# Kernel tuning notes

Hardware: AMD Instinct MI355X
Metric: run time of the kernel (lower is better)

Reference implementation:

```python
import jax, jax.numpy as jnp
import numpy as np

K = 3  # three_nn
EPS = 1e-10


def setup_inputs() -> dict:
    key = jax.random.key(0)
    ks = jax.random.split(key, 10)
    B, N, NP = 4, 16384, 4096
    C1, C2 = 128, 256
    Cin, H1, H2, Cout = C1 + C2, 256, 256, 128
    xyz1 = jax.random.normal(ks[0], (B, N, 3), dtype=jnp.float32)
    xyz2 = jax.random.normal(ks[1], (B, NP, 3), dtype=jnp.float32)
    features1 = jax.random.normal(ks[2], (B, N, C1), dtype=jnp.float32)
    features2 = jax.random.normal(ks[3], (B, NP, C2), dtype=jnp.float32)
    def lin(k, fan_in, fan_out):
        bound = 1.0 / np.sqrt(fan_in)
        kw, kb = jax.random.split(k)
        W = jax.random.uniform(kw, (fan_in, fan_out), jnp.float32, -bound, bound)
        b = jax.random.uniform(kb, (fan_out,), jnp.float32, -bound, bound)
        return W, b
    W1, b1 = lin(ks[4], Cin, H1)
    W2, b2 = lin(ks[5], H1, H2)
    W3, b3 = lin(ks[6], H2, Cout)
    return {"xyz1": xyz1, "xyz2": xyz2, "features1": features1,
            "features2": features2, "W1": W1, "b1": b1, "W2": W2,
            "b2": b2, "W3": W3, "b3": b3}


def _three_nn(xyz1, xyz2):
    # squared pairwise distances via |a|^2 + |b|^2 - 2 a.b  -> [B, N, npoint]
    sq1 = jnp.sum(xyz1 * xyz1, axis=-1)  # [B, N]
    sq2 = jnp.sum(xyz2 * xyz2, axis=-1)  # [B, npoint]
    dots = jnp.einsum("bnd,bmd->bnm", xyz1, xyz2)
    sqdist = sq1[:, :, None] + sq2[:, None, :] - 2.0 * dots
    neg_d, idx = jax.lax.top_k(-sqdist, K)  # 3 smallest squared distances
    return -neg_d, idx  # dist:[B,N,3], idx:[B,N,3]


def reference(xyz1, xyz2, features1, features2, W1, b1, W2, b2, W3, b3):
    B = xyz1.shape[0]
    dist, idx = _three_nn(xyz1, xyz2)
    # torch custom three_nn is non-differentiable in dist
    dist = jax.lax.stop_gradient(dist)
    dist = jnp.maximum(dist, EPS)
    recip = 1.0 / dist                                  # [B, N, 3]
    weight = recip / jnp.sum(recip, axis=-1, keepdims=True)
    # three_interpolate: gather neighbor features and weighted-sum
    batch_idx = jnp.arange(B)[:, None, None]
    gathered = features2[batch_idx, idx]                # [B, N, 3, C2]
    interp = jnp.einsum("bnkc,bnk->bnc", gathered, weight)
    new_features = jnp.concatenate([features1, interp], axis=-1)
    h = jax.nn.relu(new_features @ W1 + b1)
    h = jax.nn.relu(h @ W2 + b2)
    return h @ W3 + b3
```

## Files before the change

kernel.cpp:

```cpp
#include <hip/hip_runtime.h>
#include <stdint.h>

#define QT   65536
#define NPTS 4096
#define C1   128
#define C2   256
#define CIN  384
#define COUT 128

typedef _Float16 f16;
typedef __attribute__((ext_vector_type(8))) _Float16 f16x8;
typedef __attribute__((ext_vector_type(4))) float f32x4;

__device__ __attribute__((aligned(16))) f16 g_w1p[12 * 16 * 64 * 8];
__device__ __attribute__((aligned(16))) f16 g_w2p[8 * 16 * 64 * 8];
__device__ __attribute__((aligned(16))) f16 g_w3p[8 * 8 * 64 * 8];
__device__ __attribute__((aligned(16))) float4 g_cand[4 * NPTS];

__device__ inline void packW4(const float* __restrict__ W, f16* __restrict__ dst,
                              int i, int N, int NCB) {
  const int g = i & 3, quad = (i >> 2) & 3, cbk = i >> 4;
  const int cb = cbk % NCB, kcb = cbk / NCB;
  const int col = cb * 16 + g * 4;
  const int k0 = kcb * 32 + quad * 8;
  f16x8 o[4];
#pragma unroll
  for (int e = 0; e < 8; ++e) {
    float4 v = *(const float4*)(W + (size_t)(k0 + e) * N + col);
    o[0][e] = (f16)v.x; o[1][e] = (f16)v.y; o[2][e] = (f16)v.z; o[3][e] = (f16)v.w;
  }
  f16* base = dst + ((size_t)cbk * 64 + quad * 16 + g * 4) * 8;
#pragma unroll
  for (int j = 0; j < 4; ++j) *(f16x8*)(base + j * 8) = o[j];
}

__global__ __launch_bounds__(256) void prep(
    const float* __restrict__ xyz2, const float* __restrict__ W1,
    const float* __restrict__ W2,   const float* __restrict__ W3) {
  const int tid = blockIdx.x * 256 + threadIdx.x;
  const int nthr = gridDim.x * 256;
  for (int i = tid; i < 4 * NPTS; i += nthr) {
    const float* p = xyz2 + (size_t)i * 3;
    float x = p[0], y = p[1], z = p[2];
    g_cand[i] = make_float4(x, y, z, fmaf(x, x, fmaf(y, y, z * z)));
  }
  for (int i = tid; i < 12 * 16 * 16; i += nthr) packW4(W1, g_w1p, i, 256, 16);
  for (int i = tid; i < 8 * 16 * 16; i += nthr) packW4(W2, g_w2p, i, 256, 16);
  for (int i = tid; i < 8 * 8 * 16; i += nthr) packW4(W3, g_w3p, i, 128, 8);
}

__device__ inline uint32_t umin(uint32_t a, uint32_t b) { return a < b ? a : b; }
__device__ inline uint32_t med3u(uint32_t a, uint32_t b, uint32_t c) {
  uint32_t d;
  asm("v_med3_u32 %0, %1, %2, %3" : "=v"(d) : "v"(a), "v"(b), "v"(c));
  return d;
}

#define XS_STRIDE 392
#define HS_STRIDE 264
#define DMPD_OFF 16384
#define DMPI_OFF 28672
#define WV_OFF 50176
#define IV_OFF 51200
#define SMEM_BYTES 52224

__global__ __launch_bounds__(512) void fused_fp(
    const float* __restrict__ xyz1, const float* __restrict__ xyz2,
    const float* __restrict__ f1,   const float* __restrict__ f2,
    const float* __restrict__ W1,   const float* __restrict__ b1,
    const float* __restrict__ W2,   const float* __restrict__ b2,
    const float* __restrict__ W3,   const float* __restrict__ b3,
    float* __restrict__ out)
{
  __shared__ __align__(16) char smem[SMEM_BYTES];
  double*   dmpD = (double*)(smem + DMPD_OFF);
  int*      dmpI = (int*)(smem + DMPI_OFF);
  float*    wvp  = (float*)(smem + WV_OFF);
  int*      ivp  = (int*)(smem + IV_OFF);
  f16*      Xs   = (f16*)smem;
  f16*      Hs   = (f16*)smem;

  const int t = threadIdx.x;
  const int r = t & 63;
  const int w = t >> 6;
  const int qb = blockIdx.x * 64;
  const int batch = qb >> 14;
  const float* xz2b = xyz2 + (size_t)batch * NPTS * 3;
  const float* f2b  = f2   + (size_t)batch * NPTS * C2;

  const int q = qb + r;
  const float qx = xyz1[q * 3], qy = xyz1[q * 3 + 1], qz = xyz1[q * 3 + 2];
  const float nx = -2.f * qx, ny = -2.f * qy, nz = -2.f * qz;
  const float sq1q = qx * qx + qy * qy + qz * qz;

  uint32_t k0 = ~0u, k1 = ~0u, k2 = ~0u, k3 = ~0u, k4 = ~0u;

  auto ins5 = [&](uint32_t c) {
    uint32_t n0 = umin(k0, c);
    uint32_t n1 = med3u(k0, k1, c);
    uint32_t n2 = med3u(k1, k2, c);
    uint32_t n3 = med3u(k2, k3, c);
    uint32_t n4 = med3u(k3, k4, c);
    k0 = n0; k1 = n1; k2 = n2; k3 = n3; k4 = n4;
  };
  auto packk = [&](float e, uint32_t idx) -> uint32_t {
    return (__builtin_bit_cast(uint32_t, e) & 0xFFFFF000u) | idx;
  };

  {
    const int wu = __builtin_amdgcn_readfirstlane(w);
    const float4* __restrict__ cp = g_cand + (batch << 12) + (wu << 9);
    const uint32_t abase = (uint32_t)(wu << 9);
    const float sbias = sq1q + 0.05f;
    #pragma unroll 2
    for (int m = 0; m < 512; m += 4) {
      float4 c0 = cp[m], c1 = cp[m + 1], c2 = cp[m + 2], c3 = cp[m + 3];
      float e0 = fmaf(nx, c0.x, fmaf(ny, c0.y, fmaf(nz, c0.z, c0.w + sbias)));
      float e1 = fmaf(nx, c1.x, fmaf(ny, c1.y, fmaf(nz, c1.z, c1.w + sbias)));
      float e2 = fmaf(nx, c2.x, fmaf(ny, c2.y, fmaf(nz, c2.z, c2.w + sbias)));
      float e3 = fmaf(nx, c3.x, fmaf(ny, c3.y, fmaf(nz, c3.z, c3.w + sbias)));
      ins5(packk(e0, abase + m));
      ins5(packk(e1, abase + m + 1));
      ins5(packk(e2, abase + m + 2));
      ins5(packk(e3, abase + m + 3));
    }
  }

  {
    const double x1 = (double)qx, y1 = (double)qy, z1 = (double)qz;
    const double sq1 = x1 * x1 + y1 * y1 + z1 * z1;
    double d0 = 1e300, d1 = 1e300, d2 = 1e300;
    int j0 = 0, j1 = 0, j2 = 0;
    uint32_t sv[5] = {k0, k1, k2, k3, k4};
    #pragma unroll
    for (int s = 0; s < 5; ++s) {
      int idx = (int)(sv[s] & (NPTS - 1));
      const float* p2 = xz2b + (size_t)idx * 3;
      double x2 = (double)p2[0], y2 = (double)p2[1], z2 = (double)p2[2];
      double d = sq1 + (x2 * x2 + y2 * y2 + z2 * z2)
                     - 2.0 * (x1 * x2 + y1 * y2 + z1 * z2);
      bool c2 = (d < d2) || (d == d2 && idx < j2);
      bool c1 = (d < d1) || (d == d1 && idx < j1);
      bool c0 = (d < d0) || (d == d0 && idx < j0);
      d2 = c1 ? d1 : (c2 ? d : d2);  j2 = c1 ? j1 : (c2 ? idx : j2);
      d1 = c0 ? d0 : (c1 ? d : d1);  j1 = c0 ? j0 : (c1 ? idx : j1);
      d0 = c0 ? d : d0;              j0 = c0 ? idx : j0;
    }
    const int base = (w * 64 + r) * 3;
    dmpD[base]     = d0;  dmpI[base]     = j0;
    dmpD[base + 1] = d1;  dmpI[base + 1] = j1;
    dmpD[base + 2] = d2;  dmpI[base + 2] = j2;
  }
  __syncthreads();

  if (w == 0) {
    double d0 = 1e300, d1 = 1e300, d2 = 1e300;
    int j0 = 0, j1 = 0, j2 = 0;
    #pragma unroll
    for (int w2 = 0; w2 < 8; ++w2) {
      #pragma unroll
      for (int s = 0; s < 3; ++s) {
        const int base = (w2 * 64 + r) * 3 + s;
        double d = dmpD[base];
        int idx  = dmpI[base];
        bool c2 = (d < d2) || (d == d2 && idx < j2);
        bool c1 = (d < d1) || (d == d1 && idx < j1);
        bool c0 = (d < d0) || (d == d0 && idx < j0);
        d2 = c1 ? d1 : (c2 ? d : d2);  j2 = c1 ? j1 : (c2 ? idx : j2);
        d1 = c0 ? d0 : (c1 ? d : d1);  j1 = c0 ? j0 : (c1 ? idx : j1);
        d0 = c0 ? d : d0;              j0 = c0 ? idx : j0;
      }
    }
    float e0 = fmaxf((float)d0, 1e-10f);
    float e1 = fmaxf((float)d1, 1e-10f);
    float e2 = fmaxf((float)d2, 1e-10f);
    float r0 = 1.f / e0, r1 = 1.f / e1, r2 = 1.f / e2;
    float inv = 1.f / (r0 + r1 + r2);
    wvp[r * 4 + 0] = r0 * inv; wvp[r * 4 + 1] = r1 * inv;
    wvp[r * 4 + 2] = r2 * inv; wvp[r * 4 + 3] = 0.f;
    ivp[r * 4 + 0] = j0; ivp[r * 4 + 1] = j1; ivp[r * 4 + 2] = j2; ivp[r * 4 + 3] = 0;
  }
  __syncthreads();

  {
    const int row = t >> 3, c = t & 7;
    f16* xr = Xs + row * XS_STRIDE;
    {
      const float* f1r = f1 + (size_t)(qb + row) * C1 + c * 16;
      float4 u0 = *(const float4*)(f1r);
      float4 u1 = *(const float4*)(f1r + 4);
      float4 u2 = *(const float4*)(f1r + 8);
      float4 u3 = *(const float4*)(f1r + 12);
      f16x8 o0, o1;
      o0[0] = (f16)u0.x; o0[1] = (f16)u0.y; o0[2] = (f16)u0.z; o0[3] = (f16)u0.w;
      o0[4] = (f16)u1.x; o0[5] = (f16)u1.y; o0[6] = (f16)u1.z; o0[7] = (f16)u1.w;
      o1[0] = (f16)u2.x; o1[1] = (f16)u2.y; o1[2] = (f16)u2.z; o1[3] = (f16)u2.w;
      o1[4] = (f16)u3.x; o1[5] = (f16)u3.y; o1[6] = (f16)u3.z; o1[7] = (f16)u3.w;
      *(f16x8*)(xr + c * 16)     = o0;
      *(f16x8*)(xr + c * 16 + 8) = o1;
    }
    const float w0 = wvp[row * 4 + 0], w1 = wvp[row * 4 + 1], w2 = wvp[row * 4 + 2];
    const float* p0 = f2b + (size_t)(ivp[row * 4 + 0] & (NPTS - 1)) * C2;
    const float* p1 = f2b + (size_t)(ivp[row * 4 + 1] & (NPTS - 1)) * C2;
    const float* p2 = f2b + (size_t)(ivp[row * 4 + 2] & (NPTS - 1)) * C2;
    #pragma unroll
    for (int ch = 0; ch < 4; ++ch) {
      const int col = ch * 64 + c * 8;
      float4 a0 = *(const float4*)(p0 + col), b0 = *(const float4*)(p0 + col + 4);
      float4 a1 = *(const float4*)(p1 + col), b1v = *(const float4*)(p1 + col + 4);
      float4 a2 = *(const float4*)(p2 + col), b2v = *(const float4*)(p2 + col + 4);
      f16x8 o;
      o[0] = (f16)(w0 * a0.x + w1 * a1.x + w2 * a2.x);
      o[1] = (f16)(w0 * a0.y + w1 * a1.y + w2 * a2.y);
      o[2] = (f16)(w0 * a0.z + w1 * a1.z + w2 * a2.z);
      o[3] = (f16)(w0 * a0.w + w1 * a1.w + w2 * a2.w);
      o[4] = (f16)(w0 * b0.x + w1 * b1v.x + w2 * b2v.x);
      o[5] = (f16)(w0 * b0.y + w1 * b1v.y + w2 * b2v.y);
      o[6] = (f16)(w0 * b0.z + w1 * b1v.z + w2 * b2v.z);
      o[7] = (f16)(w0 * b0.w + w1 * b1v.w + w2 * b2v.w);
      *(f16x8*)(xr + C1 + col) = o;
    }
  }
  __syncthreads();

  const int l16 = r & 15, quad = r >> 4;
  const int nb = w * 32;

  f32x4 acc[4][2];
  #pragma unroll
  for (int i = 0; i < 4; ++i)
    #pragma unroll
    for (int j = 0; j < 2; ++j) acc[i][j] = f32x4{0.f, 0.f, 0.f, 0.f};

  #pragma unroll
  for (int kc = 0; kc < CIN; kc += 32) {
    f16x8 a[4];
    #pragma unroll
    for (int i = 0; i < 4; ++i)
      a[i] = *(const f16x8*)(Xs + (i * 16 + l16) * XS_STRIDE + kc + quad * 8);
    f16x8 b[2];
    #pragma unroll
    for (int j = 0; j < 2; ++j)
      b[j] = *((const f16x8*)g_w1p +
               (size_t)((kc >> 5) * 16 + (w * 2 + j)) * 64 + r);
    #pragma unroll
    for (int i = 0; i < 4; ++i)
      #pragma unroll
      for (int j = 0; j < 2; ++j)
        acc[i][j] = __builtin_amdgcn_mfma_f32_16x16x32_f16(a[i], b[j], acc[i][j], 0, 0, 0);
  }
  __syncthreads();
  #pragma unroll
  for (int j = 0; j < 2; ++j) {
    float bv = b1[nb + j * 16 + l16];
    #pragma unroll
    for (int i = 0; i < 4; ++i)
      #pragma unroll
      for (int e = 0; e < 4; ++e) {
        int row = i * 16 + quad * 4 + e;
        Hs[row * HS_STRIDE + nb + j * 16 + l16] =
            (f16)fmaxf(acc[i][j][e] + bv, 0.f);
      }
  }
  __syncthreads();

  f32x4 acc2[4][2];
  #pragma unroll
  for (int i = 0; i < 4; ++i)
    #pragma unroll
    for (int j = 0; j < 2; ++j) acc2[i][j] = f32x4{0.f, 0.f, 0.f, 0.f};

  #pragma unroll
  for (int kc = 0; kc < 256; kc += 32) {
    f16x8 a[4];
    #pragma unroll
    for (int i = 0; i < 4; ++i)
      a[i] = *(const f16x8*)(Hs + (i * 16 + l16) * HS_STRIDE + kc + quad * 8);
    f16x8 b[2];
    #pragma unroll
    for (int j = 0; j < 2; ++j)
      b[j] = *((const f16x8*)g_w2p +
               (size_t)((kc >> 5) * 16 + (w * 2 + j)) * 64 + r);
    #pragma unroll
    for (int i = 0; i < 4; ++i)
      #pragma unroll
      for (int j = 0; j < 2; ++j)
        acc2[i][j] = __builtin_amdgcn_mfma_f32_16x16x32_f16(a[i], b[j], acc2[i][j], 0, 0, 0);
  }
  __syncthreads();
  #pragma unroll
  for (int j = 0; j < 2; ++j) {
    float bv = b2[nb + j * 16 + l16];
    #pragma unroll
    for (int i = 0; i < 4; ++i)
      #pragma unroll
      for (int e = 0; e < 4; ++e) {
        int row = i * 16 + quad * 4 + e;
        Hs[row * HS_STRIDE + nb + j * 16 + l16] =
            (f16)fmaxf(acc2[i][j][e] + bv, 0.f);
      }
  }
  __syncthreads();

  const int nb3 = w * 16;
  f32x4 acc3[4];
  #pragma unroll
  for (int i = 0; i < 4; ++i) acc3[i] = f32x4{0.f, 0.f, 0.f, 0.f};

  #pragma unroll
  for (int kc = 0; kc < 256; kc += 32) {
    f16x8 a[4];
    #pragma unroll
    for (int i = 0; i < 4; ++i)
      a[i] = *(const f16x8*)(Hs + (i * 16 + l16) * HS_STRIDE + kc + quad * 8);
    f16x8 b;
    b = *((const f16x8*)g_w3p + (size_t)((kc >> 5) * 8 + w) * 64 + r);
    #pragma unroll
    for (int i = 0; i < 4; ++i)
      acc3[i] = __builtin_amdgcn_mfma_f32_16x16x32_f16(a[i], b, acc3[i], 0, 0, 0);
  }
  {
    int col = nb3 + l16;
    float bv = b3[col];
    #pragma unroll
    for (int i = 0; i < 4; ++i)
      #pragma unroll
      for (int e = 0; e < 4; ++e) {
        int row = i * 16 + quad * 4 + e;
        out[(size_t)(qb + row) * COUT + col] = acc3[i][e] + bv;
      }
  }
}

extern "C" void kernel_launch(void* const* d_in, const int* in_sizes, int n_in,
                              void* d_out, int out_size, void* d_ws, size_t ws_size,
                              hipStream_t stream)
{
  (void)out_size; (void)d_ws; (void)ws_size;
  static const int expect[10] = {196608, 49152, 8388608, 4194304,
                                 98304, 256, 65536, 256, 32768, 128};
  const void* p[10];
  bool ok = (n_in == 10);
  if (ok) {
    bool used[10] = {false};
    for (int e = 0; e < 10; ++e) {
      p[e] = nullptr;
      for (int i = 0; i < 10; ++i) {
        if (!used[i] && in_sizes[i] == expect[e]) {
          p[e] = d_in[i]; used[i] = true; break;
        }
      }
      if (!p[e]) { ok = false; break; }
    }
  }
  if (!ok)
    for (int e = 0; e < 10; ++e) p[e] = d_in[e < n_in ? e : (n_in - 1)];

  prep<<<256, 256, 0, stream>>>(
      (const float*)p[1], (const float*)p[4],
      (const float*)p[6], (const float*)p[8]);

  fused_fp<<<QT / 64, 512, 0, stream>>>(
      (const float*)p[0], (const float*)p[1],
      (const float*)p[2], (const float*)p[3],
      (const float*)p[4], (const float*)p[5],
      (const float*)p[6], (const float*)p[7],
      (const float*)p[8], (const float*)p[9],
      (float*)d_out);
}
```

Before: 213.9 us.

## Merge prep into fused kernel via grid barrier and persistent two-tile blocks

Removes the separate prep launch by having every block run a slice of the candidate and weight packing, then sync through a global atomic ticket barrier, falling back to redundant per-block prep after a spin timeout. The grid shrinks to 512 persistent blocks, each handling two 64-query tiles in a loop, with launch bounds asking for 4 blocks per CU. The goal is to save launch and inter-kernel gap overhead. The cost is a spin barrier that assumes all 512 blocks are co-resident, an extra syncthreads per tile, and possible register pressure from the occupancy hint.

```diff
diff --git a/kernel.cpp b/kernel.cpp
--- a/kernel.cpp
+++ b/kernel.cpp
@@ -7,6 +7,7 @@
 #define C2   256
 #define CIN  384
 #define COUT 128
+#define NBLK 512
 
 typedef _Float16 f16;
 typedef __attribute__((ext_vector_type(8))) _Float16 f16x8;
@@ -16,6 +17,7 @@
 __device__ __attribute__((aligned(16))) f16 g_w2p[8 * 16 * 64 * 8];
 __device__ __attribute__((aligned(16))) f16 g_w3p[8 * 8 * 64 * 8];
 __device__ __attribute__((aligned(16))) float4 g_cand[4 * NPTS];
+__device__ unsigned g_bar = 0;
 
 __device__ inline void packW4(const float* __restrict__ W, f16* __restrict__ dst,
                               int i, int N, int NCB) {
@@ -34,11 +36,11 @@
   for (int j = 0; j < 4; ++j) *(f16x8*)(base + j * 8) = o[j];
 }
 
-__global__ __launch_bounds__(256) void prep(
-    const float* __restrict__ xyz2, const float* __restrict__ W1,
-    const float* __restrict__ W2,   const float* __restrict__ W3) {
-  const int tid = blockIdx.x * 256 + threadIdx.x;
-  const int nthr = gridDim.x * 256;
+__device__ inline void prep_work(int tid, int nthr,
+                                 const float* __restrict__ xyz2,
+                                 const float* __restrict__ W1,
+                                 const float* __restrict__ W2,
+                                 const float* __restrict__ W3) {
   for (int i = tid; i < 4 * NPTS; i += nthr) {
     const float* p = xyz2 + (size_t)i * 3;
     float x = p[0], y = p[1], z = p[2];
@@ -64,7 +66,7 @@
 #define IV_OFF 51200
 #define SMEM_BYTES 52224
 
-__global__ __launch_bounds__(512) void fused_fp(
+__global__ __launch_bounds__(512, 4) void fused_all(
     const float* __restrict__ xyz1, const float* __restrict__ xyz2,
     const float* __restrict__ f1,   const float* __restrict__ f2,
     const float* __restrict__ W1,   const float* __restrict__ b1,
@@ -73,6 +75,7 @@
     float* __restrict__ out)
 {
   __shared__ __align__(16) char smem[SMEM_BYTES];
+  __shared__ int sfb;
   double*   dmpD = (double*)(smem + DMPD_OFF);
   int*      dmpI = (int*)(smem + DMPI_OFF);
   float*    wvp  = (float*)(smem + WV_OFF);
@@ -83,86 +86,85 @@
   const int t = threadIdx.x;
   const int r = t & 63;
   const int w = t >> 6;
-  const int qb = blockIdx.x * 64;
-  const int batch = qb >> 14;
-  const float* xz2b = xyz2 + (size_t)batch * NPTS * 3;
-  const float* f2b  = f2   + (size_t)batch * NPTS * C2;
-
-  const int q = qb + r;
-  const float qx = xyz1[q * 3], qy = xyz1[q * 3 + 1], qz = xyz1[q * 3 + 2];
-  const float nx = -2.f * qx, ny = -2.f * qy, nz = -2.f * qz;
-  const float sq1q = qx * qx + qy * qy + qz * qz;
-
-  uint32_t k0 = ~0u, k1 = ~0u, k2 = ~0u, k3 = ~0u, k4 = ~0u;
-
-  auto ins5 = [&](uint32_t c) {
-    uint32_t n0 = umin(k0, c);
-    uint32_t n1 = med3u(k0, k1, c);
-    uint32_t n2 = med3u(k1, k2, c);
-    uint32_t n3 = med3u(k2, k3, c);
-    uint32_t n4 = med3u(k3, k4, c);
-    k0 = n0; k1 = n1; k2 = n2; k3 = n3; k4 = n4;
-  };
-  auto packk = [&](float e, uint32_t idx) -> uint32_t {
-    return (__builtin_bit_cast(uint32_t, e) & 0xFFFFF000u) | idx;
-  };
-
-  {
-    const int wu = __builtin_amdgcn_readfirstlane(w);
-    const float4* __restrict__ cp = g_cand + (batch << 12) + (wu << 9);
-    const uint32_t abase = (uint32_t)(wu << 9);
-    const float sbias = sq1q + 0.05f;
-    #pragma unroll 2
-    for (int m = 0; m < 512; m += 4) {
-      float4 c0 = cp[m], c1 = cp[m + 1], c2 = cp[m + 2], c3 = cp[m + 3];
-      float e0 = fmaf(nx, c0.x, fmaf(ny, c0.y, fmaf(nz, c0.z, c0.w + sbias)));
-      float e1 = fmaf(nx, c1.x, fmaf(ny, c1.y, fmaf(nz, c1.z, c1.w + sbias)));
-      float e2 = fmaf(nx, c2.x, fmaf(ny, c2.y, fmaf(nz, c2.z, c2.w + sbias)));
-      float e3 = fmaf(nx, c3.x, fmaf(ny, c3.y, fmaf(nz, c3.z, c3.w + sbias)));
-      ins5(packk(e0, abase + m));
-      ins5(packk(e1, abase + m + 1));
-      ins5(packk(e2, abase + m + 2));
-      ins5(packk(e3, abase + m + 3));
-    }
-  }
-
-  {
-    const double x1 = (double)qx, y1 = (double)qy, z1 = (double)qz;
-    const double sq1 = x1 * x1 + y1 * y1 + z1 * z1;
-    double d0 = 1e300, d1 = 1e300, d2 = 1e300;
-    int j0 = 0, j1 = 0, j2 = 0;
-    uint32_t sv[5] = {k0, k1, k2, k3, k4};
-    #pragma unroll
-    for (int s = 0; s < 5; ++s) {
-      int idx = (int)(sv[s] & (NPTS - 1));
-      const float* p2 = xz2b + (size_t)idx * 3;
-      double x2 = (double)p2[0], y2 = (double)p2[1], z2 = (double)p2[2];
-      double d = sq1 + (x2 * x2 + y2 * y2 + z2 * z2)
-                     - 2.0 * (x1 * x2 + y1 * y2 + z1 * z2);
-      bool c2 = (d < d2) || (d == d2 && idx < j2);
-      bool c1 = (d < d1) || (d == d1 && idx < j1);
-      bool c0 = (d < d0) || (d == d0 && idx < j0);
-      d2 = c1 ? d1 : (c2 ? d : d2);  j2 = c1 ? j1 : (c2 ? idx : j2);
-      d1 = c0 ? d0 : (c1 ? d : d1);  j1 = c0 ? j0 : (c1 ? idx : j1);
-      d0 = c0 ? d : d0;              j0 = c0 ? idx : j0;
-    }
-    const int base = (w * 64 + r) * 3;
-    dmpD[base]     = d0;  dmpI[base]     = j0;
-    dmpD[base + 1] = d1;  dmpI[base + 1] = j1;
-    dmpD[base + 2] = d2;  dmpI[base + 2] = j2;
-  }
+
+  if (t == 0) sfb = 0;
+  prep_work(blockIdx.x * 512 + t, NBLK * 512, xyz2, W1, W2, W3);
   __syncthreads();
-
-  if (w == 0) {
-    double d0 = 1e300, d1 = 1e300, d2 = 1e300;
-    int j0 = 0, j1 = 0, j2 = 0;
-    #pragma unroll
-    for (int w2 = 0; w2 < 8; ++w2) {
-      #pragma unroll
-      for (int s = 0; s < 3; ++s) {
-        const int base = (w2 * 64 + r) * 3 + s;
-        double d = dmpD[base];
-        int idx  = dmpI[base];
+  if (t == 0) {
+    __threadfence();
+    unsigned ticket = atomicAdd(&g_bar, 1u);
+    unsigned target = (ticket / (unsigned)NBLK + 1u) * (unsigned)NBLK;
+    int spins = 0;
+    while (__hip_atomic_load(&g_bar, __ATOMIC_ACQUIRE,
+                             __HIP_MEMORY_SCOPE_AGENT) < target) {
+      if (++spins > (1 << 18)) { sfb = 1; break; }
+    }
+    __threadfence();
+  }
+  __syncthreads();
+  if (sfb) {
+    prep_work(t, 512, xyz2, W1, W2, W3);
+    __syncthreads();
+  }
+
+  #pragma unroll 1
+  for (int tile = 0; tile < 2; ++tile) {
+    const int qb = (blockIdx.x + tile * NBLK) * 64;
+    const int batch = qb >> 14;
+    const float* xz2b = xyz2 + (size_t)batch * NPTS * 3;
+    const float* f2b  = f2   + (size_t)batch * NPTS * C2;
+
+    const int q = qb + r;
+    const float qx = xyz1[q * 3], qy = xyz1[q * 3 + 1], qz = xyz1[q * 3 + 2];
+    const float nx = -2.f * qx, ny = -2.f * qy, nz = -2.f * qz;
+    const float sq1q = qx * qx + qy * qy + qz * qz;
+
+    uint32_t k0 = ~0u, k1 = ~0u, k2 = ~0u, k3 = ~0u, k4 = ~0u;
+
+    auto ins5 = [&](uint32_t c) {
+      uint32_t n0 = umin(k0, c);
+      uint32_t n1 = med3u(k0, k1, c);
+      uint32_t n2 = med3u(k1, k2, c);
+      uint32_t n3 = med3u(k2, k3, c);
+      uint32_t n4 = med3u(k3, k4, c);
+      k0 = n0; k1 = n1; k2 = n2; k3 = n3; k4 = n4;
+    };
+    auto packk = [&](float e, uint32_t idx) -> uint32_t {
+      return (__builtin_bit_cast(uint32_t, e) & 0xFFFFF000u) | idx;
+    };
+
+    {
+      const int wu = __builtin_amdgcn_readfirstlane(w);
+      const float4* __restrict__ cp = g_cand + (batch << 12) + (wu << 9);
+      const uint32_t abase = (uint32_t)(wu << 9);
+      const float sbias = sq1q + 0.05f;
+      #pragma unroll 2
+      for (int m = 0; m < 512; m += 4) {
+        float4 c0 = cp[m], c1 = cp[m + 1], c2 = cp[m + 2], c3 = cp[m + 3];
+        float e0 = fmaf(nx, c0.x, fmaf(ny, c0.y, fmaf(nz, c0.z, c0.w + sbias)));
+        float e1 = fmaf(nx, c1.x, fmaf(ny, c1.y, fmaf(nz, c1.z, c1.w + sbias)));
+        float e2 = fmaf(nx, c2.x, fmaf(ny, c2.y, fmaf(nz, c2.z, c2.w + sbias)));
+        float e3 = fmaf(nx, c3.x, fmaf(ny, c3.y, fmaf(nz, c3.z, c3.w + sbias)));
+        ins5(packk(e0, abase + m));
+        ins5(packk(e1, abase + m + 1));
+        ins5(packk(e2, abase + m + 2));
+        ins5(packk(e3, abase + m + 3));
+      }
+    }
+
+    {
+      const double x1 = (double)qx, y1 = (double)qy, z1 = (double)qz;
+      const double sq1 = x1 * x1 + y1 * y1 + z1 * z1;
+      double d0 = 1e300, d1 = 1e300, d2 = 1e300;
+      int j0 = 0, j1 = 0, j2 = 0;
+      uint32_t sv[5] = {k0, k1, k2, k3, k4};
+      #pragma unroll
+      for (int s = 0; s < 5; ++s) {
+        int idx = (int)(sv[s] & (NPTS - 1));
+        const float* p2 = xz2b + (size_t)idx * 3;
+        double x2 = (double)p2[0], y2 = (double)p2[1], z2 = (double)p2[2];
+        double d = sq1 + (x2 * x2 + y2 * y2 + z2 * z2)
+                       - 2.0 * (x1 * x2 + y1 * y2 + z1 * z2);
         bool c2 = (d < d2) || (d == d2 && idx < j2);
         bool c1 = (d < d1) || (d == d1 && idx < j1);
         bool c0 = (d < d0) || (d == d0 && idx < j0);
@@ -170,165 +172,191 @@
         d1 = c0 ? d0 : (c1 ? d : d1);  j1 = c0 ? j0 : (c1 ? idx : j1);
         d0 = c0 ? d : d0;              j0 = c0 ? idx : j0;
       }
-    }
-    float e0 = fmaxf((float)d0, 1e-10f);
-    float e1 = fmaxf((float)d1, 1e-10f);
-    float e2 = fmaxf((float)d2, 1e-10f);
-    float r0 = 1.f / e0, r1 = 1.f / e1, r2 = 1.f / e2;
-    float inv = 1.f / (r0 + r1 + r2);
-    wvp[r * 4 + 0] = r0 * inv; wvp[r * 4 + 1] = r1 * inv;
-    wvp[r * 4 + 2] = r2 * inv; wvp[r * 4 + 3] = 0.f;
-    ivp[r * 4 + 0] = j0; ivp[r * 4 + 1] = j1; ivp[r * 4 + 2] = j2; ivp[r * 4 + 3] = 0;
-  }
-  __syncthreads();
-
-  {
-    const int row = t >> 3, c = t & 7;
-    f16* xr = Xs + row * XS_STRIDE;
+      const int base = (w * 64 + r) * 3;
+      dmpD[base]     = d0;  dmpI[base]     = j0;
+      dmpD[base + 1] = d1;  dmpI[base + 1] = j1;
+      dmpD[base + 2] = d2;  dmpI[base + 2] = j2;
+    }
+    __syncthreads();
+
+    if (w == 0) {
+      double d0 = 1e300, d1 = 1e300, d2 = 1e300;
+      int j0 = 0, j1 = 0, j2 = 0;
+      #pragma unroll
+      for (int w2 = 0; w2 < 8; ++w2) {
+        #pragma unroll
+        for (int s = 0; s < 3; ++s) {
+          const int base = (w2 * 64 + r) * 3 + s;
+          double d = dmpD[base];
+          int idx  = dmpI[base];
+          bool c2 = (d < d2) || (d == d2 && idx < j2);
+          bool c1 = (d < d1) || (d == d1 && idx < j1);
+          bool c0 = (d < d0) || (d == d0 && idx < j0);
+          d2 = c1 ? d1 : (c2 ? d : d2);  j2 = c1 ? j1 : (c2 ? idx : j2);
+          d1 = c0 ? d0 : (c1 ? d : d1);  j1 = c0 ? j0 : (c1 ? idx : j1);
+          d0 = c0 ? d : d0;              j0 = c0 ? idx : j0;
+        }
+      }
+      float e0 = fmaxf((float)d0, 1e-10f);
+      float e1 = fmaxf((float)d1, 1e-10f);
+      float e2 = fmaxf((float)d2, 1e-10f);
+      float r0 = 1.f / e0, r1 = 1.f / e1, r2 = 1.f / e2;
+      float inv = 1.f / (r0 + r1 + r2);
+      wvp[r * 4 + 0] = r0 * inv; wvp[r * 4 + 1] = r1 * inv;
+      wvp[r * 4 + 2] = r2 * inv; wvp[r * 4 + 3] = 0.f;
+      ivp[r * 4 + 0] = j0; ivp[r * 4 + 1] = j1; ivp[r * 4 + 2] = j2; ivp[r * 4 + 3] = 0;
+    }
+    __syncthreads();
+
     {
-      const float* f1r = f1 + (size_t)(qb + row) * C1 + c * 16;
-      float4 u0 = *(const float4*)(f1r);
-      float4 u1 = *(const float4*)(f1r + 4);
-      float4 u2 = *(const float4*)(f1r + 8);
-      float4 u3 = *(const float4*)(f1r + 12);
-      f16x8 o0, o1;
-      o0[0] = (f16)u0.x; o0[1] = (f16)u0.y; o0[2] = (f16)u0.z; o0[3] = (f16)u0.w;
-      o0[4] = (f16)u1.x; o0[5] = (f16)u1.y; o0[6] = (f16)u1.z; o0[7] = (f16)u1.w;
-      o1[0] = (f16)u2.x; o1[1] = (f16)u2.y; o1[2] = (f16)u2.z; o1[3] = (f16)u2.w;
-      o1[4] = (f16)u3.x; o1[5] = (f16)u3.y; o1[6] = (f16)u3.z; o1[7] = (f16)u3.w;
-      *(f16x8*)(xr + c * 16)     = o0;
-      *(f16x8*)(xr + c * 16 + 8) = o1;
-    }
-    const float w0 = wvp[row * 4 + 0], w1 = wvp[row * 4 + 1], w2 = wvp[row * 4 + 2];
-    const float* p0 = f2b + (size_t)(ivp[row * 4 + 0] & (NPTS - 1)) * C2;
-    const float* p1 = f2b + (size_t)(ivp[row * 4 + 1] & (NPTS - 1)) * C2;
-    const float* p2 = f2b + (size_t)(ivp[row * 4 + 2] & (NPTS - 1)) * C2;
-    #pragma unroll
-    for (int ch = 0; ch < 4; ++ch) {
-      const int col = ch * 64 + c * 8;
-      float4 a0 = *(const float4*)(p0 + col), b0 = *(const float4*)(p0 + col + 4);
-      float4 a1 = *(const float4*)(p1 + col), b1v = *(const float4*)(p1 + col + 4);
-      float4 a2 = *(const float4*)(p2 + col), b2v = *(const float4*)(p2 + col + 4);
-      f16x8 o;
-      o[0] = (f16)(w0 * a0.x + w1 * a1.x + w2 * a2.x);
-      o[1] = (f16)(w0 * a0.y + w1 * a1.y + w2 * a2.y);
-      o[2] = (f16)(w0 * a0.z + w1 * a1.z + w2 * a2.z);
-      o[3] = (f16)(w0 * a0.w + w1 * a1.w + w2 * a2.w);
-      o[4] = (f16)(w0 * b0.x + w1 * b1v.x + w2 * b2v.x);
-      o[5] = (f16)(w0 * b0.y + w1 * b1v.y + w2 * b2v.y);
-      o[6] = (f16)(w0 * b0.z + w1 * b1v.z + w2 * b2v.z);
-      o[7] = (f16)(w0 * b0.w + w1 * b1v.w + w2 * b2v.w);
-      *(f16x8*)(xr + C1 + col) = o;
-    }
-  }
-  __syncthreads();
-
-  const int l16 = r & 15, quad = r >> 4;
-  const int nb = w * 32;
-
-  f32x4 acc[4][2];
-  #pragma unroll
-  for (int i = 0; i < 4; ++i)
-    #pragma unroll
-    for (int j = 0; j < 2; ++j) acc[i][j] = f32x4{0.f, 0.f, 0.f, 0.f};
-
-  #pragma unroll
-  for (int kc = 0; kc < CIN; kc += 32) {
-    f16x8 a[4];
+      const int row = t >> 3, c = t & 7;
+      f16* xr = Xs + row * XS_STRIDE;
+      {
+        const float* f1r = f1 + (size_t)(qb + row) * C1 + c * 16;
+        float4 u0 = *(const float4*)(f1r);
+        float4 u1 = *(const float4*)(f1r + 4);
+        float4 u2 = *(const float4*)(f1r + 8);
+        float4 u3 = *(const float4*)(f1r + 12);
+        f16x8 o0, o1;
+        o0[0] = (f16)u0.x; o0[1] = (f16)u0.y; o0[2] = (f16)u0.z; o0[3] = (f16)u0.w;
+        o0[4] = (f16)u1.x; o0[5] = (f16)u1.y; o0[6] = (f16)u1.z; o0[7] = (f16)u1.w;
+        o1[0] = (f16)u2.x; o1[1] = (f16)u2.y; o1[2] = (f16)u2.z; o1[3] = (f16)u2.w;
+        o1[4] = (f16)u3.x; o1[5] = (f16)u3.y; o1[6] = (f16)u3.z; o1[7] = (f16)u3.w;
+        *(f16x8*)(xr + c * 16)     = o0;
+        *(f16x8*)(xr + c * 16 + 8) = o1;
+      }
+      const float w0 = wvp[row * 4 + 0], w1 = wvp[row * 4 + 1], w2 = wvp[row * 4 + 2];
+      const float* p0 = f2b + (size_t)(ivp[row * 4 + 0] & (NPTS - 1)) * C2;
+      const float* p1 = f2b + (size_t)(ivp[row * 4 + 1] & (NPTS - 1)) * C2;
+      const float* p2 = f2b + (size_t)(ivp[row * 4 + 2] & (NPTS - 1)) * C2;
+      #pragma unroll
+      for (int ch = 0; ch < 4; ++ch) {
+        const int col = ch * 64 + c * 8;
+        float4 a0 = *(const float4*)(p0 + col), b0 = *(const float4*)(p0 + col + 4);
+        float4 a1 = *(const float4*)(p1 + col), b1v = *(const float4*)(p1 + col + 4);
+        float4 a2 = *(const float4*)(p2 + col), b2v = *(const float4*)(p2 + col + 4);
+        f16x8 o;
+        o[0] = (f16)(w0 * a0.x + w1 * a1.x + w2 * a2.x);
+        o[1] = (f16)(w0 * a0.y + w1 * a1.y + w2 * a2.y);
+        o[2] = (f16)(w0 * a0.z + w1 * a1.z + w2 * a2.z);
+        o[3] = (f16)(w0 * a0.w + w1 * a1.w + w2 * a2.w);
+        o[4] = (f16)(w0 * b0.x + w1 * b1v.x + w2 * b2v.x);
+        o[5] = (f16)(w0 * b0.y + w1 * b1v.y + w2 * b2v.y);
+        o[6] = (f16)(w0 * b0.z + w1 * b1v.z + w2 * b2v.z);
+        o[7] = (f16)(w0 * b0.w + w1 * b1v.w + w2 * b2v.w);
+        *(f16x8*)(xr + C1 + col) = o;
+      }
+    }
+    __syncthreads();
+
+    const int l16 = r & 15, quad = r >> 4;
+    const int nb = w * 32;
+
+    f32x4 acc[4][2];
     #pragma unroll
     for (int i = 0; i < 4; ++i)
-      a[i] = *(const f16x8*)(Xs + (i * 16 + l16) * XS_STRIDE + kc + quad * 8);
-    f16x8 b[2];
-    #pragma unroll
-    for (int j = 0; j < 2; ++j)
-      b[j] = *((const f16x8*)g_w1p +
-               (size_t)((kc >> 5) * 16 + (w * 2 + j)) * 64 + r);
+      #pragma unroll
+      for (int j = 0; j < 2; ++j) acc[i][j] = f32x4{0.f, 0.f, 0.f, 0.f};
+
+    #pragma unroll
+    for (int kc = 0; kc < CIN; kc += 32) {
+      f16x8 a[4];
+      #pragma unroll
+      for (int i = 0; i < 4; ++i)
+        a[i] = *(const f16x8*)(Xs + (i * 16 + l16) * XS_STRIDE + kc + quad * 8);
+      f16x8 b[2];
+      #pragma unroll
+      for (int j = 0; j < 2; ++j)
+        b[j] = *((const f16x8*)g_w1p +
+                 (size_t)((kc >> 5) * 16 + (w * 2 + j)) * 64 + r);
+      #pragma unroll
+      for (int i = 0; i < 4; ++i)
+        #pragma unroll
+        for (int j = 0; j < 2; ++j)
+          acc[i][j] = __builtin_amdgcn_mfma_f32_16x16x32_f16(a[i], b[j], acc[i][j], 0, 0, 0);
+    }
+    __syncthreads();
+    #pragma unroll
+    for (int j = 0; j < 2; ++j) {
+      float bv = b1[nb + j * 16 + l16];
+      #pragma unroll
+      for (int i = 0; i < 4; ++i)
+        #pragma unroll
+        for (int e = 0; e < 4; ++e) {
+          int row = i * 16 + quad * 4 + e;
+          Hs[row * HS_STRIDE + nb + j * 16 + l16] =
+              (f16)fmaxf(acc[i][j][e] + bv, 0.f);
+        }
+    }
+    __syncthreads();
+
+    f32x4 acc2[4][2];
     #pragma unroll
     for (int i = 0; i < 4; ++i)
       #pragma unroll
+      for (int j = 0; j < 2; ++j) acc2[i][j] = f32x4{0.f, 0.f, 0.f, 0.f};
+
+    #pragma unroll
+    for (int kc = 0; kc < 256; kc += 32) {
+      f16x8 a[4];
+      #pragma unroll
+      for (int i = 0; i < 4; ++i)
+        a[i] = *(const f16x8*)(Hs + (i * 16 + l16) * HS_STRIDE + kc + quad * 8);
+      f16x8 b[2];
+      #pragma unroll
       for (int j = 0; j < 2; ++j)
-        acc[i][j] = __builtin_amdgcn_mfma_f32_16x16x32_f16(a[i], b[j], acc[i][j], 0, 0, 0);
-  }
-  __syncthreads();
-  #pragma unroll
-  for (int j = 0; j < 2; ++j) {
-    float bv = b1[nb + j * 16 + l16];
-    #pragma unroll
-    for (int i = 0; i < 4; ++i)
-      #pragma unroll
-      for (int e = 0; e < 4; ++e) {
-        int row = i * 16 + quad * 4 + e;
-        Hs[row * HS_STRIDE + nb + j * 16 + l16] =
-            (f16)fmaxf(acc[i][j][e] + bv, 0.f);
-      }
-  }
-  __syncthreads();
-
-  f32x4 acc2[4][2];
-  #pragma unroll
-  for (int i = 0; i < 4; ++i)
-    #pragma unroll
-    for (int j = 0; j < 2; ++j) acc2[i][j] = f32x4{0.f, 0.f, 0.f, 0.f};
-
-  #pragma unroll
-  for (int kc = 0; kc < 256; kc += 32) {
-    f16x8 a[4];
-    #pragma unroll
-    for (int i = 0; i < 4; ++i)
-      a[i] = *(const f16x8*)(Hs + (i * 16 + l16) * HS_STRIDE + kc + quad * 8);
-    f16x8 b[2];
-    #pragma unroll
-    for (int j = 0; j < 2; ++j)
-      b[j] = *((const f16x8*)g_w2p +
-               (size_t)((kc >> 5) * 16 + (w * 2 + j)) * 64 + r);
-    #pragma unroll
-    for (int i = 0; i < 4; ++i)
-      #pragma unroll
-      for (int j = 0; j < 2; ++j)
-        acc2[i][j] = __builtin_amdgcn_mfma_f32_16x16x32_f16(a[i], b[j], acc2[i][j], 0, 0, 0);
-  }
-  __syncthreads();
-  #pragma unroll
-  for (int j = 0; j < 2; ++j) {
-    float bv = b2[nb + j * 16 + l16];
-    #pragma unroll
-    for (int i = 0; i < 4; ++i)
-      #pragma unroll
-      for (int e = 0; e < 4; ++e) {
-        int row = i * 16 + quad * 4 + e;
-        Hs[row * HS_STRIDE + nb + j * 16 + l16] =
-            (f16)fmaxf(acc2[i][j][e] + bv, 0.f);
-      }
-  }
-  __syncthreads();
-
-  const int nb3 = w * 16;
-  f32x4 acc3[4];
-  #pragma unroll
-  for (int i = 0; i < 4; ++i) acc3[i] = f32x4{0.f, 0.f, 0.f, 0.f};
-
-  #pragma unroll
-  for (int kc = 0; kc < 256; kc += 32) {
-    f16x8 a[4];
-    #pragma unroll
-    for (int i = 0; i < 4; ++i)
-      a[i] = *(const f16x8*)(Hs + (i * 16 + l16) * HS_STRIDE + kc + quad * 8);
-    f16x8 b;
-    b = *((const f16x8*)g_w3p + (size_t)((kc >> 5) * 8 + w) * 64 + r);
-    #pragma unroll
-    for (int i = 0; i < 4; ++i)
-      acc3[i] = __builtin_amdgcn_mfma_f32_16x16x32_f16(a[i], b, acc3[i], 0, 0, 0);
-  }
-  {
-    int col = nb3 + l16;
-    float bv = b3[col];
-    #pragma unroll
-    for (int i = 0; i < 4; ++i)
-      #pragma unroll
-      for (int e = 0; e < 4; ++e) {
-        int row = i * 16 + quad * 4 + e;
-        out[(size_t)(qb + row) * COUT + col] = acc3[i][e] + bv;
-      }
+        b[j] = *((const f16x8*)g_w2p +
+                 (size_t)((kc >> 5) * 16 + (w * 2 + j)) * 64 + r);
+      #pragma unroll
+      for (int i = 0; i < 4; ++i)
+        #pragma unroll
+        for (int j = 0; j < 2; ++j)
+          acc2[i][j] = __builtin_amdgcn_mfma_f32_16x16x32_f16(a[i], b[j], acc2[i][j], 0, 0, 0);
+    }
+    __syncthreads();
+    #pragma unroll
+    for (int j = 0; j < 2; ++j) {
+      float bv = b2[nb + j * 16 + l16];
+      #pragma unroll
+      for (int i = 0; i < 4; ++i)
+        #pragma unroll
+        for (int e = 0; e < 4; ++e) {
+          int row = i * 16 + quad * 4 + e;
+          Hs[row * HS_STRIDE + nb + j * 16 + l16] =
+              (f16)fmaxf(acc2[i][j][e] + bv, 0.f);
+        }
+    }
+    __syncthreads();
+
+    const int nb3 = w * 16;
+    f32x4 acc3[4];
+    #pragma unroll
+    for (int i = 0; i < 4; ++i) acc3[i] = f32x4{0.f, 0.f, 0.f, 0.f};
+
+    #pragma unroll
+    for (int kc = 0; kc < 256; kc += 32) {
+      f16x8 a[4];
+      #pragma unroll
+      for (int i = 0; i < 4; ++i)
+        a[i] = *(const f16x8*)(Hs + (i * 16 + l16) * HS_STRIDE + kc + quad * 8);
+      f16x8 b;
+      b = *((const f16x8*)g_w3p + (size_t)((kc >> 5) * 8 + w) * 64 + r);
+      #pragma unroll
+      for (int i = 0; i < 4; ++i)
+        acc3[i] = __builtin_amdgcn_mfma_f32_16x16x32_f16(a[i], b, acc3[i], 0, 0, 0);
+    }
+    {
+      int col = nb3 + l16;
+      float bv = b3[col];
+      #pragma unroll
+      for (int i = 0; i < 4; ++i)
+        #pragma unroll
+        for (int e = 0; e < 4; ++e) {
+          int row = i * 16 + quad * 4 + e;
+          out[(size_t)(qb + row) * COUT + col] = acc3[i][e] + bv;
+        }
+    }
+    __syncthreads();
   }
 }
 
@@ -356,11 +384,7 @@
   if (!ok)
     for (int e = 0; e < 10; ++e) p[e] = d_in[e < n_in ? e : (n_in - 1)];
 
-  prep<<<256, 256, 0, stream>>>(
-      (const float*)p[1], (const float*)p[4],
-      (const float*)p[6], (const float*)p[8]);
-
-  fused_fp<<<QT / 64, 512, 0, stream>>>(
+  fused_all<<<NBLK, 512, 0, stream>>>(
       (const float*)p[0], (const float*)p[1],
       (const float*)p[2], (const float*)p[3],
       (const float*)p[4], (const float*)p[5],
```

Result: slower. 393.5 us (+83.9%).
